# Kernel tuning notes

Measured on AMD Instinct MI355X. Metric: run time of the kernel, lower is better.

## Reference

```python
import jax, jax.numpy as jnp
import numpy as np

B, Tc, E, K, M, V = 8, 1024, 256, 8, 2048, 16
T1 = Tc * K          # penultimate layer length = 8192
TLAST = M * K        # last layer length = 16384


def setup_inputs() -> dict:
    key = jax.random.key(0)
    ks = jax.random.split(key, 12)
    x = jax.random.normal(ks[0], (B, Tc, E), jnp.float32)
    # penultimate values: exactly M 'mixed' tokens (value==2) per row, rest in {1,3}
    base = jnp.where(jnp.arange(T1) < M, 2, 1 + 2 * jax.random.randint(ks[1], (B, T1), 0, 2))
    perm = jnp.argsort(jax.random.uniform(ks[2], (B, T1)), axis=1)
    val1 = jnp.take_along_axis(base, perm, axis=1)
    vallast = 1 + 2 * jax.random.randint(ks[3], (B, TLAST), 0, 2)
    value = jnp.concatenate([val1, vallast], axis=1).astype(jnp.int64)
    depth = jnp.concatenate([jnp.full((B, T1), 5), jnp.full((B, TLAST), 6)], axis=1).astype(jnp.int64)
    pos = jax.random.randint(ks[4], (B, T1 + TLAST, 3), 0, 64).astype(jnp.int64)
    s = 0.02
    W1 = s * jax.random.normal(ks[5], (E, E, K), jnp.float32)  # ConvTranspose1d weight [in,out,k]
    b1 = s * jax.random.normal(ks[6], (E,), jnp.float32)
    W0 = s * jax.random.normal(ks[7], (E, E, K), jnp.float32)
    b0 = s * jax.random.normal(ks[8], (E,), jnp.float32)
    Wl = s * jax.random.normal(ks[9], (V + 1, E), jnp.float32)
    bl = s * jax.random.normal(ks[10], (V + 1,), jnp.float32)
    return {"x": x, "value": value, "depth": depth, "pos": pos, "num_mix": M,
            "W1": W1, "b1": b1, "W0": W0, "b0": b0, "Wl": Wl, "bl": bl}


def _deconv(x, W, b):
    # ConvTranspose1d with kernel=stride=K: each token expands to K tokens
    n, t, e = x.shape
    o = W.shape[1]
    y = jnp.einsum('nte,eoj->ntjo', x, W)  # [N,T,K,O]
    return y.reshape(n, t * W.shape[2], o) + b


def reference(x, value, depth, pos, num_mix, W1, b1, W0, b0, Wl, bl):
    n, tc, e = x.shape
    k = W1.shape[2]
    t1 = tc * k
    max_depth = jnp.max(depth)
    len_1 = jnp.sum(depth == max_depth - 1, axis=1)               # [N]
    tt = jnp.arange(t1)
    val_1 = jnp.where(tt[None, :] < len_1[:, None], value[:, :t1], 0)  # padded penultimate values
    mix_mask = val_1 == 2                                         # [N,T1]
    mix_1 = jnp.sum(mix_mask, axis=1)                             # [N]
    y_1 = _deconv(x, W1, b1)                                      # [N,T1,E]
    # stable pack: bring positions with value==2 to the front, keep order
    order = jnp.argsort(jnp.where(mix_mask, 0, 1), axis=1, stable=True)
    sel = order[:, :num_mix]                                      # [N,M]
    x_0 = jnp.take_along_axis(y_1, sel[:, :, None], axis=1)       # [N,M,E]
    valid = (jnp.arange(num_mix)[None, :] < mix_1[:, None]).astype(x_0.dtype)
    x_0 = x_0 * valid[:, :, None]                                 # zero-pad beyond per-row mix count
    y_0 = _deconv(x_0, W0, b0)                                    # [N,M*K,E]
    return y_0 @ Wl.T + bl                                        # [N,M*K,V+1]
```

## Files before the change

### kernel.cpp

```cpp
#include <hip/hip_runtime.h>

typedef __attribute__((ext_vector_type(8))) short bf16x8;
typedef __attribute__((ext_vector_type(4))) float f32x4;

#define BB 8
#define TC 1024
#define EE 256
#define KJ 8
#define MSEL 2048
#define V1 17
#define T1 8192
#define TTOT 24576
#define BI_TOT 16384
#define NCOLP 160
#define WSTRIDE 264

#define SCAL_OFF 0
#define GRP_OFF  1024
#define WFT_OFF  (GRP_OFF + 524288)
#define B2_OFF   (WFT_OFF + NCOLP*WSTRIDE*2)
#define BF0_OFF  (B2_OFF + 640)
#define WCT_OFF  (BF0_OFF + 128)

__device__ __forceinline__ unsigned short f2bf(float f) {
    union { float f; unsigned u; } x; x.f = f;
    unsigned r = x.u + 0x7fffu + ((x.u >> 16) & 1u);
    return (unsigned short)(r >> 16);
}
__device__ __forceinline__ float bf2f(unsigned short h) {
    union { unsigned u; float f; } x; x.u = ((unsigned)h) << 16;
    return x.f;
}

__device__ __forceinline__ float blockReduceSum256(float v) {
    __shared__ float sm[4];
    #pragma unroll
    for (int d = 32; d; d >>= 1) v += __shfl_down(v, d, 64);
    int lane = threadIdx.x & 63, wid = threadIdx.x >> 6;
    if (lane == 0) sm[wid] = v;
    __syncthreads();
    float r = sm[0] + sm[1] + sm[2] + sm[3];
    __syncthreads();
    return r;
}

__global__ __launch_bounds__(256) void k_pre(const float* W0, const float* Wl, const int* depth,
                                             unsigned short* wfT, int* scal) {
    int bid = blockIdx.x, tid = threadIdx.x;
    __shared__ float w0s[EE * KJ];
    __shared__ float wls[V1 * 257];
    __shared__ int s_red[4];
    if (bid < 256) {
        int em = bid;
        for (int idx = tid; idx < EE * KJ; idx += 256) w0s[idx] = W0[em * EE * KJ + idx];
        for (int idx = tid; idx < V1 * EE; idx += 256) {
            int v = idx >> 8, o = idx & 255;
            wls[v * 257 + o] = Wl[idx];
        }
        __syncthreads();
        if (tid < 136) {
            int j = tid / V1, v = tid - j * V1;
            float acc = 0.f;
            #pragma unroll 4
            for (int o = 0; o < EE; ++o) acc += w0s[o * KJ + j] * wls[v * 257 + o];
            wfT[(j * 20 + v) * WSTRIDE + em] = f2bf(acc);
        }
    } else {
        int b = bid - 256;
        if (b == 0 && tid < 8) scal[33 + tid] = 0;
        const int4* dp = (const int4*)(depth + b * TTOT);
        int m = -2147483648;
        for (int i = tid; i < 6144; i += 256) {
            int4 d = dp[i];
            m = max(max(m, max(d.x, d.y)), max(d.z, d.w));
        }
        #pragma unroll
        for (int dd = 32; dd; dd >>= 1) m = max(m, __shfl_down(m, dd, 64));
        if ((tid & 63) == 0) s_red[tid >> 6] = m;
        __syncthreads();
        int bmax = max(max(s_red[0], s_red[1]), max(s_red[2], s_red[3]));
        if (tid == 0) { atomicMax(&scal[0], bmax); scal[1 + b] = bmax; }
        int c1 = 0, c2 = 0;
        for (int i = tid; i < 6144; i += 256) {
            int4 d = dp[i];
            c1 += (d.x == bmax) + (d.y == bmax) + (d.z == bmax) + (d.w == bmax);
            c2 += (d.x == bmax - 1) + (d.y == bmax - 1) + (d.z == bmax - 1) + (d.w == bmax - 1);
        }
        int cc = (c1 << 16) + c2;
        #pragma unroll
        for (int dd = 32; dd; dd >>= 1) cc += __shfl_down(cc, dd, 64);
        __syncthreads();
        if ((tid & 63) == 0) s_red[tid >> 6] = cc;
        __syncthreads();
        if (tid == 0) {
            int tot = s_red[0] + s_red[1] + s_red[2] + s_red[3];
            scal[9 + b] = tot >> 16;
            scal[17 + b] = tot & 0xffff;
        }
    }
}

__global__ __launch_bounds__(256) void k_mid(
        const int* value, const float* W1, const float* b1, const float* b0,
        const float* Wl, const float* bl,
        int* scal, int* groups, const unsigned short* wfT, float* bias2, float* bf0,
        unsigned short* wct) {
    int bid = blockIdx.x, tid = threadIdx.x;
    __shared__ union {
        struct { unsigned short b1s[32 * WSTRIDE]; unsigned short af[NCOLP * 72]; } w;
    } sm;
    __shared__ int s_wt[4], s_lcnt[8], s_lcnt2[8], s_lbase[8];
    if (bid < 64) {
        int g = bid >> 3;
        int e0 = (bid & 7) * 32;
        unsigned short* b1s = sm.w.b1s;
        unsigned short* af = sm.w.af;
        {
            int em_l = tid & 63;
            int eb = (tid >> 6) * 8;
            #pragma unroll
            for (int i = 0; i < 8; ++i) {
                int e = eb + i;
                #pragma unroll
                for (int c = 0; c < 4; ++c) {
                    int em = c * 64 + em_l;
                    b1s[e * WSTRIDE + em] = f2bf(W1[(e0 + e) * (EE * KJ) + em * KJ + g]);
                }
            }
        }
        for (int idx = tid; idx < 1280; idx += 256) {
            int row = idx >> 3, f = idx & 7;
            ((int4*)af)[row * 9 + f] = ((const int4*)wfT)[row * 33 + f];
        }
        __syncthreads();

        int w = tid >> 6, l = tid & 63;
        int ntile = w & 1, mhalf = w >> 1;
        int lr = l & 15, lq = l >> 4;
        f32x4 acc[5];
        #pragma unroll
        for (int t = 0; t < 5; ++t) acc[t] = (f32x4){0.f, 0.f, 0.f, 0.f};

        for (int ch = 0; ch < 4; ++ch) {
            if (ch) {
                __syncthreads();
                for (int idx = tid; idx < 1280; idx += 256) {
                    int row = idx >> 3, f = idx & 7;
                    ((int4*)af)[row * 9 + f] = ((const int4*)wfT)[row * 33 + ch * 8 + f];
                }
                __syncthreads();
            }
            #pragma unroll
            for (int s = 0; s < 2; ++s) {
                bf16x8 bfr = *(const bf16x8*)&b1s[(ntile * 16 + lr) * WSTRIDE + ch * 64 + s * 32 + lq * 8];
                #pragma unroll
                for (int t = 0; t < 5; ++t) {
                    bf16x8 afr = *(const bf16x8*)&af[((mhalf * 5 + t) * 16 + lr) * 72 + s * 32 + lq * 8];
                    acc[t] = __builtin_amdgcn_mfma_f32_16x16x32_bf16(afr, bfr, acc[t], 0, 0, 0);
                }
            }
        }
        #pragma unroll
        for (int t = 0; t < 5; ++t) {
            int m = (mhalf * 5 + t) * 16 + lq * 4;
            int n = e0 + ntile * 16 + lr;
            #pragma unroll
            for (int r = 0; r < 4; ++r)
                wct[(g * NCOLP + m + r) * WSTRIDE + n] = f2bf(acc[t][r]);
        }
    } else if (bid < 72) {
        int b = bid - 64;
        int gmax = scal[0];
        int mb = scal[1 + b], cm = scal[9 + b], cm1 = scal[17 + b];
        int len1 = (mb == gmax) ? cm1 : ((mb == gmax - 1) ? cm : 0);
        const int* vb = value + b * TTOT;
        int t0 = tid * 32;
        unsigned mask = 0;
        #pragma unroll
        for (int k = 0; k < 32; k += 4) {
            int4 v = *(const int4*)(vb + t0 + k);
            if (t0 + k + 0 < len1 && v.x == 2) mask |= 1u << (k + 0);
            if (t0 + k + 1 < len1 && v.y == 2) mask |= 1u << (k + 1);
            if (t0 + k + 2 < len1 && v.z == 2) mask |= 1u << (k + 2);
            if (t0 + k + 3 < len1 && v.w == 2) mask |= 1u << (k + 3);
        }
        int cnt = __popc(mask);
        int inc = cnt;
        #pragma unroll
        for (int d = 1; d < 64; d <<= 1) {
            int n = __shfl_up(inc, d, 64);
            if ((tid & 63) >= d) inc += n;
        }
        int lane = tid & 63, wid = tid >> 6;
        if (lane == 63) s_wt[wid] = inc;
        if (tid < 8) { s_lcnt[tid] = 0; s_lcnt2[tid] = 0; }
        __syncthreads();
        int woff = 0;
        for (int w = 0; w < wid; ++w) woff += s_wt[w];
        int off0 = woff + inc - cnt;
        int mix1 = s_wt[0] + s_wt[1] + s_wt[2] + s_wt[3];
        int mix1c = min(mix1, MSEL);
        {
            int off = off0;
            #pragma unroll
            for (int k = 0; k < 32; ++k) {
                if (mask & (1u << k)) {
                    if (off < MSEL) atomicAdd(&s_lcnt[(t0 + k) & 7], 1);
                    off++;
                }
            }
        }
        if (tid == 0 && mix1c < MSEL) atomicAdd(&s_lcnt[0], MSEL - mix1c);
        __syncthreads();
        if (tid < 8) s_lbase[tid] = atomicAdd(&scal[33 + tid], s_lcnt[tid]);
        __syncthreads();
        {
            int off = off0;
            #pragma unroll
            for (int k = 0; k < 32; ++k) {
                if (mask & (1u << k)) {
                    if (off < MSEL) {
                        int t = t0 + k;
                        int g = t & 7;
                        int ls = atomicAdd(&s_lcnt2[g], 1);
                        groups[g * BI_TOT + s_lbase[g] + ls] =
                            ((b * MSEL + off) << 11) | ((t >> 3) << 1) | 1;
                    }
                    off++;
                }
            }
        }
        for (int i = mix1c + tid; i < MSEL; i += 256) {
            int ls = atomicAdd(&s_lcnt2[0], 1);
            groups[s_lbase[0] + ls] = (b * MSEL + i) << 11;
        }
    } else if (bid < 89) {
        int v = bid - 72;
        float s = blockReduceSum256(b0[tid] * Wl[v * EE + tid]);
        if (tid == 0) bf0[v] = s + bl[v];
    } else {
        #pragma unroll
        for (int r = 0; r < 2; ++r) {
            int c17 = (bid - 89) * 2 + r;
            int j = c17 / V1, v = c17 - j * V1;
            int colP = j * 20 + v;
            float s = blockReduceSum256(b1[tid] * bf2f(wfT[colP * WSTRIDE + tid]));
            if (tid == 0) bias2[colP] = s;
        }
    }
}

__global__ __launch_bounds__(256) void k_main(const float* x, const unsigned short* wct,
        const int* scal, const int* groups, const float* bias2, const float* bf0, float* out) {
    int g = blockIdx.x >> 7;
    int tile0 = blockIdx.x & 127;
    int cntg = scal[33 + g];

    __shared__ __align__(16) unsigned short xs[32 * WSTRIDE];
    __shared__ __align__(16) unsigned short wts[NCOLP * 72];
    __shared__ int xoffs[32], obase[32];
    __shared__ unsigned char vflag[32];
    int tid = threadIdx.x;
    const int4* wsrc = (const int4*)wct;

    for (int tile = tile0; tile * 32 < cntg; tile += 128) {
        int nrows = min(32, cntg - tile * 32);
        __syncthreads();
        if (tid < 32) {
            int flag = 0, xo = 0, ob = 0;
            if (tid < nrows) {
                int p = groups[g * BI_TOT + tile * 32 + tid];
                int valid = p & 1;
                int tq = (p >> 1) & 1023;
                int bi = p >> 11;
                int b = bi >> 11;
                xo = (b * TC + tq) * EE;
                ob = bi * 136;
                flag = 1 + valid;
            }
            xoffs[tid] = xo; obase[tid] = ob; vflag[tid] = (unsigned char)flag;
        }
        __syncthreads();
        {
            int row = tid >> 3, q = tid & 7;
            const float* xp = x + xoffs[row];
            #pragma unroll
            for (int i = 0; i < 8; ++i) {
                int f4 = q + 8 * i;
                float4 v = *(const float4*)(xp + f4 * 4);
                ushort4 pk;
                pk.x = f2bf(v.x); pk.y = f2bf(v.y); pk.z = f2bf(v.z); pk.w = f2bf(v.w);
                *(ushort4*)&xs[row * WSTRIDE + f4 * 4] = pk;
            }
        }
        for (int idx = tid; idx < 1280; idx += 256) {
            int row = idx >> 3, f = idx & 7;
            ((int4*)wts)[row * 9 + f] = wsrc[(g * NCOLP + row) * 33 + f];
        }
        __syncthreads();

        int w = tid >> 6, l = tid & 63;
        int rw = w & 1, chalf = w >> 1;
        int lr = l & 15, lq = l >> 4;
        f32x4 acc[5];
        #pragma unroll
        for (int t = 0; t < 5; ++t) acc[t] = (f32x4){0.f, 0.f, 0.f, 0.f};

        for (int ch = 0; ch < 4; ++ch) {
            if (ch) {
                __syncthreads();
                for (int idx = tid; idx < 1280; idx += 256) {
                    int row = idx >> 3, f = idx & 7;
                    ((int4*)wts)[row * 9 + f] = wsrc[(g * NCOLP + row) * 33 + ch * 8 + f];
                }
                __syncthreads();
            }
            #pragma unroll
            for (int s = 0; s < 2; ++s) {
                bf16x8 afr = *(const bf16x8*)&xs[(rw * 16 + lr) * WSTRIDE + ch * 64 + s * 32 + lq * 8];
                #pragma unroll
                for (int t = 0; t < 5; ++t) {
                    bf16x8 bfr = *(const bf16x8*)&wts[((chalf * 5 + t) * 16 + lr) * 72 + s * 32 + lq * 8];
                    acc[t] = __builtin_amdgcn_mfma_f32_16x16x32_bf16(afr, bfr, acc[t], 0, 0, 0);
                }
            }
        }
        #pragma unroll
        for (int t = 0; t < 5; ++t) {
            int col = (chalf * 5 + t) * 16 + lr;
            int j = col / 20, v = col % 20;
            if (v < V1) {
                float bb = bias2[col] + bf0[v];
                float b0v = bf0[v];
                #pragma unroll
                for (int r = 0; r < 4; ++r) {
                    int row = rw * 16 + lq * 4 + r;
                    int fl = vflag[row];
                    if (fl) out[obase[row] + j * V1 + v] = (fl == 2) ? (acc[t][r] + bb) : b0v;
                }
            }
        }
    }
}

extern "C" void kernel_launch(void* const* d_in, const int* in_sizes, int n_in,
                              void* d_out, int out_size, void* d_ws, size_t ws_size,
                              hipStream_t stream) {
    const float* x     = (const float*)d_in[0];
    const int*   value = (const int*)d_in[1];
    const int*   depth = (const int*)d_in[2];
    const float* W1    = (const float*)d_in[5];
    const float* b1    = (const float*)d_in[6];
    const float* W0    = (const float*)d_in[7];
    const float* b0    = (const float*)d_in[8];
    const float* Wl    = (const float*)d_in[9];
    const float* bl    = (const float*)d_in[10];
    float* out = (float*)d_out;
    char* ws = (char*)d_ws;

    int*            scal   = (int*)(ws + SCAL_OFF);
    int*            groups = (int*)(ws + GRP_OFF);
    unsigned short* wfT    = (unsigned short*)(ws + WFT_OFF);
    float*          bias2  = (float*)(ws + B2_OFF);
    float*          bf0    = (float*)(ws + BF0_OFF);
    unsigned short* wct    = (unsigned short*)(ws + WCT_OFF);

    k_pre <<<dim3(264),  dim3(256), 0, stream>>>(W0, Wl, depth, wfT, scal);
    k_mid <<<dim3(157),  dim3(256), 0, stream>>>(value, W1, b1, b0, Wl, bl,
                                                 scal, groups, wfT, bias2, bf0, wct);
    k_main<<<dim3(1024), dim3(256), 0, stream>>>(x, wct, scal, groups, bias2, bf0, out);
}
```

Baseline: 115.2 us.

## Keep full weight tile resident in LDS and prefetch next x tile in registers

k_main now loads the whole 160x256 per-group weight tile into shared memory once, instead of re-staging 64-column chunks with extra barriers each tile. It uses 256 persistent blocks that prefetch the next tile's x rows into registers with double-buffered row metadata while the current tile computes. k_pre folds the depth-reduction blocks into the weight-product blocks and drops the atomicMax; k_mid recomputes the global max from per-batch maxima and computes bias2/bf0 in blocks 0/1. The aim is fewer launches and blocks, fewer barriers and overlap of global loads with MFMA work, at the cost of much larger LDS use per block and less parallelism.

```diff
diff --git a/kernel.cpp b/kernel.cpp
--- a/kernel.cpp
+++ b/kernel.cpp
@@ -32,41 +32,28 @@
     return x.f;
 }
 
-__device__ __forceinline__ float blockReduceSum256(float v) {
-    __shared__ float sm[4];
-    #pragma unroll
-    for (int d = 32; d; d >>= 1) v += __shfl_down(v, d, 64);
-    int lane = threadIdx.x & 63, wid = threadIdx.x >> 6;
-    if (lane == 0) sm[wid] = v;
-    __syncthreads();
-    float r = sm[0] + sm[1] + sm[2] + sm[3];
-    __syncthreads();
-    return r;
-}
-
 __global__ __launch_bounds__(256) void k_pre(const float* W0, const float* Wl, const int* depth,
                                              unsigned short* wfT, int* scal) {
     int bid = blockIdx.x, tid = threadIdx.x;
     __shared__ float w0s[EE * KJ];
     __shared__ float wls[V1 * 257];
     __shared__ int s_red[4];
-    if (bid < 256) {
-        int em = bid;
-        for (int idx = tid; idx < EE * KJ; idx += 256) w0s[idx] = W0[em * EE * KJ + idx];
-        for (int idx = tid; idx < V1 * EE; idx += 256) {
-            int v = idx >> 8, o = idx & 255;
-            wls[v * 257 + o] = Wl[idx];
-        }
-        __syncthreads();
-        if (tid < 136) {
-            int j = tid / V1, v = tid - j * V1;
-            float acc = 0.f;
-            #pragma unroll 4
-            for (int o = 0; o < EE; ++o) acc += w0s[o * KJ + j] * wls[v * 257 + o];
-            wfT[(j * 20 + v) * WSTRIDE + em] = f2bf(acc);
-        }
-    } else {
-        int b = bid - 256;
+    int em = bid;
+    for (int idx = tid; idx < EE * KJ; idx += 256) w0s[idx] = W0[em * EE * KJ + idx];
+    for (int idx = tid; idx < V1 * EE; idx += 256) {
+        int v = idx >> 8, o = idx & 255;
+        wls[v * 257 + o] = Wl[idx];
+    }
+    __syncthreads();
+    if (tid < 136) {
+        int j = tid / V1, v = tid - j * V1;
+        float acc = 0.f;
+        #pragma unroll 4
+        for (int o = 0; o < EE; ++o) acc += w0s[o * KJ + j] * wls[v * 257 + o];
+        wfT[(j * 20 + v) * WSTRIDE + em] = f2bf(acc);
+    }
+    if (bid < 8) {
+        int b = bid;
         if (b == 0 && tid < 8) scal[33 + tid] = 0;
         const int4* dp = (const int4*)(depth + b * TTOT);
         int m = -2147483648;
@@ -79,7 +66,7 @@
         if ((tid & 63) == 0) s_red[tid >> 6] = m;
         __syncthreads();
         int bmax = max(max(s_red[0], s_red[1]), max(s_red[2], s_red[3]));
-        if (tid == 0) { atomicMax(&scal[0], bmax); scal[1 + b] = bmax; }
+        if (tid == 0) scal[1 + b] = bmax;
         int c1 = 0, c2 = 0;
         for (int i = tid; i < 6144; i += 256) {
             int4 d = dp[i];
@@ -106,15 +93,12 @@
         int* scal, int* groups, const unsigned short* wfT, float* bias2, float* bf0,
         unsigned short* wct) {
     int bid = blockIdx.x, tid = threadIdx.x;
-    __shared__ union {
-        struct { unsigned short b1s[32 * WSTRIDE]; unsigned short af[NCOLP * 72]; } w;
-    } sm;
+    __shared__ __align__(16) unsigned short b1s[32 * WSTRIDE];
+    __shared__ __align__(16) unsigned short af[NCOLP * WSTRIDE];
     __shared__ int s_wt[4], s_lcnt[8], s_lcnt2[8], s_lbase[8];
     if (bid < 64) {
         int g = bid >> 3;
         int e0 = (bid & 7) * 32;
-        unsigned short* b1s = sm.w.b1s;
-        unsigned short* af = sm.w.af;
         {
             int em_l = tid & 63;
             int eb = (tid >> 6) * 8;
@@ -128,9 +112,9 @@
                 }
             }
         }
-        for (int idx = tid; idx < 1280; idx += 256) {
-            int row = idx >> 3, f = idx & 7;
-            ((int4*)af)[row * 9 + f] = ((const int4*)wfT)[row * 33 + f];
+        for (int idx = tid; idx < 5120; idx += 256) {
+            int row = idx >> 5, f = idx & 31;
+            ((int4*)af)[row * 33 + f] = ((const int4*)wfT)[row * 33 + f];
         }
         __syncthreads();
 
@@ -141,21 +125,14 @@
         #pragma unroll
         for (int t = 0; t < 5; ++t) acc[t] = (f32x4){0.f, 0.f, 0.f, 0.f};
 
+        #pragma unroll
         for (int ch = 0; ch < 4; ++ch) {
-            if (ch) {
-                __syncthreads();
-                for (int idx = tid; idx < 1280; idx += 256) {
-                    int row = idx >> 3, f = idx & 7;
-                    ((int4*)af)[row * 9 + f] = ((const int4*)wfT)[row * 33 + ch * 8 + f];
-                }
-                __syncthreads();
-            }
             #pragma unroll
             for (int s = 0; s < 2; ++s) {
                 bf16x8 bfr = *(const bf16x8*)&b1s[(ntile * 16 + lr) * WSTRIDE + ch * 64 + s * 32 + lq * 8];
                 #pragma unroll
                 for (int t = 0; t < 5; ++t) {
-                    bf16x8 afr = *(const bf16x8*)&af[((mhalf * 5 + t) * 16 + lr) * 72 + s * 32 + lq * 8];
+                    bf16x8 afr = *(const bf16x8*)&af[((mhalf * 5 + t) * 16 + lr) * WSTRIDE + ch * 64 + s * 32 + lq * 8];
                     acc[t] = __builtin_amdgcn_mfma_f32_16x16x32_bf16(afr, bfr, acc[t], 0, 0, 0);
                 }
             }
@@ -168,10 +145,34 @@
             for (int r = 0; r < 4; ++r)
                 wct[(g * NCOLP + m + r) * WSTRIDE + n] = f2bf(acc[t][r]);
         }
-    } else if (bid < 72) {
+        if (bid == 0) {
+            for (int c = tid; c < NCOLP; c += 256) {
+                int vv = c % 20;
+                float s = 0.f;
+                if (vv < V1) {
+                    for (int e8 = 0; e8 < 32; ++e8) {
+                        bf16x8 a8 = *(const bf16x8*)&af[c * WSTRIDE + e8 * 8];
+                        #pragma unroll
+                        for (int u = 0; u < 8; ++u)
+                            s += b1[e8 * 8 + u] * bf2f((unsigned short)a8[u]);
+                    }
+                }
+                bias2[c] = s;
+            }
+        } else if (bid == 1) {
+            if (tid < V1) {
+                float s = 0.f;
+                #pragma unroll 4
+                for (int e = 0; e < EE; ++e) s += b0[e] * Wl[tid * EE + e];
+                bf0[tid] = s + bl[tid];
+            }
+        }
+    } else {
         int b = bid - 64;
-        int gmax = scal[0];
         int mb = scal[1 + b], cm = scal[9 + b], cm1 = scal[17 + b];
+        int gmax = scal[1];
+        #pragma unroll
+        for (int q = 2; q <= 8; ++q) gmax = max(gmax, scal[q]);
         int len1 = (mb == gmax) ? cm1 : ((mb == gmax - 1) ? cm : 0);
         const int* vb = value + b * TTOT;
         int t0 = tid * 32;
@@ -234,93 +235,96 @@
             int ls = atomicAdd(&s_lcnt2[0], 1);
             groups[s_lbase[0] + ls] = (b * MSEL + i) << 11;
         }
-    } else if (bid < 89) {
-        int v = bid - 72;
-        float s = blockReduceSum256(b0[tid] * Wl[v * EE + tid]);
-        if (tid == 0) bf0[v] = s + bl[v];
-    } else {
-        #pragma unroll
-        for (int r = 0; r < 2; ++r) {
-            int c17 = (bid - 89) * 2 + r;
-            int j = c17 / V1, v = c17 - j * V1;
-            int colP = j * 20 + v;
-            float s = blockReduceSum256(b1[tid] * bf2f(wfT[colP * WSTRIDE + tid]));
-            if (tid == 0) bias2[colP] = s;
-        }
     }
 }
 
 __global__ __launch_bounds__(256) void k_main(const float* x, const unsigned short* wct,
         const int* scal, const int* groups, const float* bias2, const float* bf0, float* out) {
-    int g = blockIdx.x >> 7;
-    int tile0 = blockIdx.x & 127;
+    int g = blockIdx.x >> 5;
+    int slot = blockIdx.x & 31;
     int cntg = scal[33 + g];
+    if (slot * 32 >= cntg) return;
 
     __shared__ __align__(16) unsigned short xs[32 * WSTRIDE];
-    __shared__ __align__(16) unsigned short wts[NCOLP * 72];
-    __shared__ int xoffs[32], obase[32];
-    __shared__ unsigned char vflag[32];
+    __shared__ __align__(16) unsigned short wts[NCOLP * WSTRIDE];
+    __shared__ int xoffs[2][32], obase[2][32];
+    __shared__ unsigned char vflag[2][32];
     int tid = threadIdx.x;
     const int4* wsrc = (const int4*)wct;
 
-    for (int tile = tile0; tile * 32 < cntg; tile += 128) {
-        int nrows = min(32, cntg - tile * 32);
-        __syncthreads();
-        if (tid < 32) {
+    if (tid < 32) {
+        int nrows = min(32, cntg - slot * 32);
+        int flag = 0, xo = 0, ob = 0;
+        if (tid < nrows) {
+            int pk = groups[g * BI_TOT + slot * 32 + tid];
+            int tq = (pk >> 1) & 1023;
+            int bi = pk >> 11;
+            xo = ((bi >> 11) * TC + tq) * EE;
+            ob = bi * 136;
+            flag = 1 + (pk & 1);
+        }
+        xoffs[0][tid] = xo; obase[0][tid] = ob; vflag[0][tid] = (unsigned char)flag;
+    }
+    for (int idx = tid; idx < 5120; idx += 256) {
+        int row = idx >> 5, f = idx & 31;
+        ((int4*)wts)[row * 33 + f] = wsrc[(g * NCOLP + row) * 33 + f];
+    }
+    __syncthreads();
+
+    int w = tid >> 6, l = tid & 63;
+    int rw = w & 1, chalf = w >> 1;
+    int lr = l & 15, lq = l >> 4;
+    int row8 = tid >> 3, q8 = tid & 7;
+
+    float4 xr[8];
+    {
+        const float* xp = x + xoffs[0][row8];
+        #pragma unroll
+        for (int i = 0; i < 8; ++i) xr[i] = *(const float4*)(xp + (q8 + 8 * i) * 4);
+    }
+
+    int pp = 0;
+    for (int tile = slot; tile * 32 < cntg; tile += 32, pp ^= 1) {
+        #pragma unroll
+        for (int i = 0; i < 8; ++i) {
+            ushort4 pk;
+            pk.x = f2bf(xr[i].x); pk.y = f2bf(xr[i].y);
+            pk.z = f2bf(xr[i].z); pk.w = f2bf(xr[i].w);
+            *(ushort4*)&xs[row8 * WSTRIDE + (q8 + 8 * i) * 4] = pk;
+        }
+        int ntile = tile + 32;
+        int more = (ntile * 32 < cntg);
+        if (more && tid < 32) {
+            int nrows = min(32, cntg - ntile * 32);
             int flag = 0, xo = 0, ob = 0;
             if (tid < nrows) {
-                int p = groups[g * BI_TOT + tile * 32 + tid];
-                int valid = p & 1;
-                int tq = (p >> 1) & 1023;
-                int bi = p >> 11;
-                int b = bi >> 11;
-                xo = (b * TC + tq) * EE;
+                int pk = groups[g * BI_TOT + ntile * 32 + tid];
+                int tq = (pk >> 1) & 1023;
+                int bi = pk >> 11;
+                xo = ((bi >> 11) * TC + tq) * EE;
                 ob = bi * 136;
-                flag = 1 + valid;
-            }
-            xoffs[tid] = xo; obase[tid] = ob; vflag[tid] = (unsigned char)flag;
-        }
-        __syncthreads();
-        {
-            int row = tid >> 3, q = tid & 7;
-            const float* xp = x + xoffs[row];
-            #pragma unroll
-            for (int i = 0; i < 8; ++i) {
-                int f4 = q + 8 * i;
-                float4 v = *(const float4*)(xp + f4 * 4);
-                ushort4 pk;
-                pk.x = f2bf(v.x); pk.y = f2bf(v.y); pk.z = f2bf(v.z); pk.w = f2bf(v.w);
-                *(ushort4*)&xs[row * WSTRIDE + f4 * 4] = pk;
-            }
-        }
-        for (int idx = tid; idx < 1280; idx += 256) {
-            int row = idx >> 3, f = idx & 7;
-            ((int4*)wts)[row * 9 + f] = wsrc[(g * NCOLP + row) * 33 + f];
-        }
-        __syncthreads();
-
-        int w = tid >> 6, l = tid & 63;
-        int rw = w & 1, chalf = w >> 1;
-        int lr = l & 15, lq = l >> 4;
+                flag = 1 + (pk & 1);
+            }
+            xoffs[pp ^ 1][tid] = xo; obase[pp ^ 1][tid] = ob; vflag[pp ^ 1][tid] = (unsigned char)flag;
+        }
+        __syncthreads();
+        if (more) {
+            const float* xp = x + xoffs[pp ^ 1][row8];
+            #pragma unroll
+            for (int i = 0; i < 8; ++i) xr[i] = *(const float4*)(xp + (q8 + 8 * i) * 4);
+        }
+
         f32x4 acc[5];
         #pragma unroll
         for (int t = 0; t < 5; ++t) acc[t] = (f32x4){0.f, 0.f, 0.f, 0.f};
-
+        #pragma unroll
         for (int ch = 0; ch < 4; ++ch) {
-            if (ch) {
-                __syncthreads();
-                for (int idx = tid; idx < 1280; idx += 256) {
-                    int row = idx >> 3, f = idx & 7;
-                    ((int4*)wts)[row * 9 + f] = wsrc[(g * NCOLP + row) * 33 + ch * 8 + f];
-                }
-                __syncthreads();
-            }
             #pragma unroll
             for (int s = 0; s < 2; ++s) {
                 bf16x8 afr = *(const bf16x8*)&xs[(rw * 16 + lr) * WSTRIDE + ch * 64 + s * 32 + lq * 8];
                 #pragma unroll
                 for (int t = 0; t < 5; ++t) {
-                    bf16x8 bfr = *(const bf16x8*)&wts[((chalf * 5 + t) * 16 + lr) * 72 + s * 32 + lq * 8];
+                    bf16x8 bfr = *(const bf16x8*)&wts[((chalf * 5 + t) * 16 + lr) * WSTRIDE + ch * 64 + s * 32 + lq * 8];
                     acc[t] = __builtin_amdgcn_mfma_f32_16x16x32_bf16(afr, bfr, acc[t], 0, 0, 0);
                 }
             }
@@ -335,11 +339,12 @@
                 #pragma unroll
                 for (int r = 0; r < 4; ++r) {
                     int row = rw * 16 + lq * 4 + r;
-                    int fl = vflag[row];
-                    if (fl) out[obase[row] + j * V1 + v] = (fl == 2) ? (acc[t][r] + bb) : b0v;
-                }
-            }
-        }
+                    int fl = vflag[pp][row];
+                    if (fl) out[obase[pp][row] + j * V1 + v] = (fl == 2) ? (acc[t][r] + bb) : b0v;
+                }
+            }
+        }
+        __syncthreads();
     }
 }
 
@@ -365,8 +370,8 @@
     float*          bf0    = (float*)(ws + BF0_OFF);
     unsigned short* wct    = (unsigned short*)(ws + WCT_OFF);
 
-    k_pre <<<dim3(264),  dim3(256), 0, stream>>>(W0, Wl, depth, wfT, scal);
-    k_mid <<<dim3(157),  dim3(256), 0, stream>>>(value, W1, b1, b0, Wl, bl,
-                                                 scal, groups, wfT, bias2, bf0, wct);
-    k_main<<<dim3(1024), dim3(256), 0, stream>>>(x, wct, scal, groups, bias2, bf0, out);
-}
+    k_pre <<<dim3(256), dim3(256), 0, stream>>>(W0, Wl, depth, wfT, scal);
+    k_mid <<<dim3(72),  dim3(256), 0, stream>>>(value, W1, b1, b0, Wl, bl,
+                                                scal, groups, wfT, bias2, bf0, wct);
+    k_main<<<dim3(256), dim3(256), 0, stream>>>(x, wct, scal, groups, bias2, bf0, out);
+}
```

Measured after the change: 131.8 us. 1.14x slower.
